# Optimization experiments

Hardware: AMD Instinct MI355X
Metric: run time of the kernel (lower is better)

Reference implementation:

```python
import jax, jax.numpy as jnp
import numpy as np
import math

N_CELLS = 16384
INPUT_DIM = 512
HIDDEN = 512


def build_neighbors(n):
    n_bits = max(1, int(math.ceil(math.log2(n))))
    idx = np.arange(n)
    flips = [idx ^ (1 << b) for b in range(n_bits)]
    ring = [(idx + 1) % n, (idx - 1) % n]
    allnb = np.stack(flips + ring, axis=1)
    # dedupe per row; for power-of-2 n every row has exactly n_bits+1 uniques
    rows = [sorted(set(r.tolist())) for r in allnb]
    return np.asarray(rows, dtype=np.int32)


def setup_inputs() -> dict:
    key = jax.random.key(0)
    ks = jax.random.split(key, 12)
    n, d, h = N_CELLS, INPUT_DIM, HIDDEN
    amp = jax.random.uniform(ks[0], (n, h)) * 0.5 + 0.5
    phase = jax.random.normal(ks[1], (n, h)) * 0.3 + (2 * math.pi * jnp.arange(n) / n)[:, None]
    return {
        "x": jax.random.normal(ks[2], (1, d), dtype=jnp.float32),
        "pump_W": jax.random.normal(ks[3], (n, d), dtype=jnp.float32) / np.sqrt(d),
        "pump_b": jax.random.normal(ks[4], (n,), dtype=jnp.float32) * 0.01,
        "dec_W": jax.random.normal(ks[5], (d, 2 * h), dtype=jnp.float32) / np.sqrt(2 * h),
        "dec_b": jax.random.normal(ks[6], (d,), dtype=jnp.float32) * 0.01,
        "cs_re": (amp * jnp.cos(phase)).astype(jnp.float32),
        "cs_im": (amp * jnp.sin(phase)).astype(jnp.float32),
        "excited": jax.random.uniform(ks[7], (n,)) * 0.6,  # some cells above 0.5 threshold
        "phase_vel": jax.random.normal(ks[8], (n, h), dtype=jnp.float32) * 0.05,
        "cav_re": jax.random.normal(ks[9], (h,), dtype=jnp.float32) * 0.01,
        "cav_im": jax.random.normal(ks[10], (h,), dtype=jnp.float32) * 0.01,
        "neighbors": jnp.asarray(build_neighbors(n)),
    }


def reference(x, pump_W, pump_b, dec_W, dec_b, cs_re, cs_im, excited, phase_vel, cav_re, cav_im, neighbors):
    states = (cs_re + 1j * cs_im).astype(jnp.complex64)          # [n,h]
    cavity = (cav_re + 1j * cav_im).astype(jnp.complex64)        # [h]

    # pump + excited fraction update
    pump = jax.nn.sigmoid(x @ pump_W.T + pump_b)[0]              # [n]
    excited = jnp.clip(excited * 0.95 + pump * 0.05, 0.0, 1.0)

    # free phase rotation: polar(1, 0.1*phase_vel)
    states = states * jnp.exp(1j * (phase_vel * 0.1)).astype(jnp.complex64)

    # neighbor phase coupling (hypercube + ring, k=15 neighbors each)
    ang = jnp.angle(states)                                      # [n,h]
    nb_states = states[neighbors]                                # [n,k,h]
    coupling = jnp.cos(ang[:, None, :] - ang[neighbors])         # [n,k,h]
    interference = 0.1 * jnp.sum(coupling * nb_states, axis=1)   # [n,h]
    k = neighbors.shape[1]
    new_states = 0.7 * states + 0.3 * interference / k

    # lasing: population inversion threshold
    lasing = excited > 0.5                                       # [n]
    n_lasing = jnp.sum(lasing)
    maskf = lasing.astype(jnp.float32)[:, None]
    # emission uses pre-phase-lock states (torch copies lasing_cells first)
    emission = jnp.sum(new_states * maskf, axis=0) / jnp.maximum(n_lasing, 1).astype(jnp.float32)
    cavity_new = jnp.where(n_lasing > 0, 0.8 * cavity + 0.2 * emission, cavity)

    # phase-lock lasing cells to (old) cavity phase
    cavity_phase = jnp.angle(cavity)                             # old cavity
    new_ang = jnp.angle(new_states)
    locked = 0.3 * cavity_phase[None, :] + 0.7 * new_ang
    locked_states = jnp.abs(new_states) * jnp.exp(1j * locked)
    new_states = jnp.where(lasing[:, None], locked_states.astype(jnp.complex64), new_states)
    excited = jnp.where(lasing, excited * 0.9, excited * 0.98)

    # cavity feedback (updated cavity) + amplitude renorm
    new_states = new_states + 0.05 * cavity_new[None, :]
    amp = jnp.abs(new_states)
    amp = amp / (jnp.max(amp, axis=-1, keepdims=True) + 1e-8)
    final_states = (amp * jnp.exp(1j * jnp.angle(new_states))).astype(jnp.complex64)

    # decode cavity mode
    out_real = jnp.concatenate([cavity_new.real, cavity_new.imag])[None, :].astype(jnp.float32)  # [1,2h]
    pred = out_real @ dec_W.T + dec_b                            # [1, input_dim]
    tension = jnp.var(jnp.abs(final_states))
    return pred, tension
```

## Files before the change

kernel.cpp:

```cpp
#include <hip/hip_runtime.h>
#include <hip/hip_fp16.h>
#include <math.h>

#define N_CELLS 16384
#define HID 512
#define IND 512
#define KNB 15
#define NCOPY 64

#define ROT_BLOCKS  8192
#define PUMP_BLOCKS 4096
#define ZERO_BLOCKS 64

#define CPB 32
#define CELL_BLOCKS (N_CELLS / CPB)
#define PRED_BLOCKS 128

#define CNT_OFF   0
#define EMIS_OFF  128
#define LAS_OFF   (EMIS_OFF + NCOPY*1024*4)
#define VPART_OFF (LAS_OFF + N_CELLS*4)
#define ROT_OFF   (1<<20)
#define NST_OFF   (ROT_OFF + (size_t)N_CELLS*HID*4)

__device__ inline __half2 f2h2(float f) { union { float f; __half2 h; } u; u.f = f; return u.h; }
__device__ inline float   h22f(__half2 h) { union { float f; __half2 h; } u; u.h = h; return u.f; }

__global__ __launch_bounds__(256) void k_front(const float* __restrict__ cr,
                                               const float* __restrict__ ci,
                                               const float* __restrict__ pv,
                                               float4* __restrict__ rot,
                                               const float* __restrict__ x,
                                               const float* __restrict__ pW,
                                               const float* __restrict__ pb,
                                               const float* __restrict__ excited,
                                               int* __restrict__ lasing,
                                               float* __restrict__ emis,
                                               int* __restrict__ cnt) {
    int b = blockIdx.x;
    int tid = threadIdx.x;
    if (b < ROT_BLOCKS) {
        int i = b * 256 + tid;
        const float4* cr4 = (const float4*)cr;
        const float4* ci4 = (const float4*)ci;
        const float4* pv4 = (const float4*)pv;
        float4 a = cr4[i], bb = ci4[i], t = pv4[i];
        float s0, c0, s1, c1, s2, c2, s3, c3;
        __sincosf(0.1f * t.x, &s0, &c0);
        __sincosf(0.1f * t.y, &s1, &c1);
        __sincosf(0.1f * t.z, &s2, &c2);
        __sincosf(0.1f * t.w, &s3, &c3);
        float re0 = a.x * c0 - bb.x * s0, im0 = a.x * s0 + bb.x * c0;
        float re1 = a.y * c1 - bb.y * s1, im1 = a.y * s1 + bb.y * c1;
        float re2 = a.z * c2 - bb.z * s2, im2 = a.z * s2 + bb.z * c2;
        float re3 = a.w * c3 - bb.w * s3, im3 = a.w * s3 + bb.w * c3;
        rot[i] = make_float4(h22f(__floats2half2_rn(re0, re1)),
                             h22f(__floats2half2_rn(im0, im1)),
                             h22f(__floats2half2_rn(re2, re3)),
                             h22f(__floats2half2_rn(im2, im3)));
    } else if (b < ROT_BLOCKS + PUMP_BLOCKS) {
        int gtid = (b - ROT_BLOCKS) * 256 + tid;
        int cell = gtid >> 6;
        int lane = gtid & 63;
        const float4* w4 = (const float4*)(pW + (size_t)cell * IND);
        const float4* x4 = (const float4*)x;
        float acc = 0.f;
#pragma unroll
        for (int t = 0; t < (IND / 4) / 64; ++t) {
            float4 a = w4[lane + 64 * t];
            float4 bx = x4[lane + 64 * t];
            acc += a.x * bx.x + a.y * bx.y + a.z * bx.z + a.w * bx.w;
        }
#pragma unroll
        for (int o = 32; o; o >>= 1) acc += __shfl_xor(acc, o, 64);
        if (lane == 0) {
            float p = 1.f / (1.f + expf(-(acc + pb[cell])));
            float e = excited[cell] * 0.95f + p * 0.05f;
            e = fminf(fmaxf(e, 0.f), 1.f);
            lasing[cell] = (e > 0.5f) ? 1 : 0;
        }
    } else {
        int zb = b - ROT_BLOCKS - PUMP_BLOCKS;
        int idx = zb * 256 + tid;
        ((float4*)emis)[idx] = make_float4(0.f, 0.f, 0.f, 0.f);
        if (zb == 0 && tid == 0) *cnt = 0;
    }
}

__global__ __launch_bounds__(256) void k_coup(const float2* __restrict__ rot2,
                                              const int* __restrict__ nbrs,
                                              const int* __restrict__ lasing,
                                              float2* __restrict__ nst2,
                                              float* __restrict__ emis) {
    __shared__ int nb[KNB];
    __shared__ int las;
    int cell = blockIdx.x;
    int tid = threadIdx.x;
    if (tid < KNB) nb[tid] = nbrs[cell * KNB + tid];
    if (tid == KNB) las = lasing[cell];
    __syncthreads();

    float2 raw = rot2[(size_t)cell * (HID / 2) + tid];
    __half2 sre = f2h2(raw.x), sim = f2h2(raw.y);
    float s0x = __low2float(sre), s1x = __high2float(sre);
    float s0y = __low2float(sim), s1y = __high2float(sim);
    float r0 = rsqrtf(s0x * s0x + s0y * s0y);
    float r1 = rsqrtf(s1x * s1x + s1y * s1y);

    __half2 are = __float2half2_rn(0.f), aim = __float2half2_rn(0.f);
#pragma unroll
    for (int t = 0; t < KNB; ++t) {
        float2 qraw = rot2[(size_t)nb[t] * (HID / 2) + tid];
        __half2 qre = f2h2(qraw.x), qim = f2h2(qraw.y);
        __half2 d  = __hfma2(sim, qim, __hmul2(sre, qre));
        __half2 qn = __hfma2(qim, qim, __hmul2(qre, qre));
        __half2 t2 = __hmul2(d, h2rsqrt(qn));
        are = __hfma2(t2, qre, are);
        aim = __hfma2(t2, qim, aim);
    }
    float ar0 = __low2float(are), ar1 = __high2float(are);
    float ai0 = __low2float(aim), ai1 = __high2float(aim);
    float k0 = 0.002f * r0, k1 = 0.002f * r1;
    float nr0 = 0.7f * s0x + k0 * ar0, ni0 = 0.7f * s0y + k0 * ai0;
    float nr1 = 0.7f * s1x + k1 * ar1, ni1 = 0.7f * s1y + k1 * ai1;
    nst2[(size_t)cell * (HID / 2) + tid] =
        make_float2(h22f(__floats2half2_rn(nr0, nr1)),
                    h22f(__floats2half2_rn(ni0, ni1)));
    if (las) {
        int c0 = tid << 1;
        float* em = emis + (size_t)(cell & (NCOPY - 1)) * 1024;
        atomicAdd(em + c0,     nr0); atomicAdd(em + 512 + c0,     ni0);
        atomicAdd(em + c0 + 1, nr1); atomicAdd(em + 512 + c0 + 1, ni1);
    }
}

__global__ __launch_bounds__(256) void k_finall(const float2* __restrict__ nst2,
                                                const int* __restrict__ lasv,
                                                const float* __restrict__ emis,
                                                const float* __restrict__ cavr,
                                                const float* __restrict__ cavi,
                                                const float* __restrict__ dW,
                                                const float* __restrict__ db,
                                                float2* __restrict__ vpart,
                                                int* __restrict__ cnt,
                                                float* __restrict__ out) {
    __shared__ float sout[1024];
    __shared__ float sphase[512];
    __shared__ int   ic[4];
    __shared__ int   snl;
    __shared__ float sred[4];
    __shared__ float sbc;
    __shared__ float w1[4], w2[4];
    __shared__ int   slast;

    int t = threadIdx.x;
    int wid = t >> 6, lane = t & 63;

    const int4* l4 = (const int4*)lasv;
    int n = 0;
#pragma unroll
    for (int k = 0; k < N_CELLS / 4 / 256; ++k) {
        int4 v = l4[t + 256 * k];
        n += v.x + v.y + v.z + v.w;
    }
#pragma unroll
    for (int o = 32; o; o >>= 1) n += __shfl_xor(n, o, 64);
    if (lane == 0) ic[wid] = n;

    float4 acc = make_float4(0.f, 0.f, 0.f, 0.f);
    const float4* e4 = (const float4*)emis;
#pragma unroll 8
    for (int k = 0; k < NCOPY; ++k) {
        float4 v = e4[k * 256 + t];
        acc.x += v.x; acc.y += v.y; acc.z += v.z; acc.w += v.w;
    }
    __syncthreads();
    if (t == 0) snl = ic[0] + ic[1] + ic[2] + ic[3];
    __syncthreads();
    int nl = snl;

    const float4* cr4 = (const float4*)cavr;
    const float4* ci4 = (const float4*)cavi;
    float4 cv = (t < 128) ? cr4[t] : ci4[t - 128];
    float4 nv;
    if (nl > 0) {
        float inv = 0.2f / (float)(nl > 1 ? nl : 1);
        nv = make_float4(0.8f * cv.x + acc.x * inv, 0.8f * cv.y + acc.y * inv,
                         0.8f * cv.z + acc.z * inv, 0.8f * cv.w + acc.w * inv);
    } else {
        nv = cv;
    }
    ((float4*)sout)[t] = nv;
    if (t < 128) {
        float4 cr = cr4[t], ci = ci4[t];
        sphase[4 * t]     = atan2f(ci.x, cr.x);
        sphase[4 * t + 1] = atan2f(ci.y, cr.y);
        sphase[4 * t + 2] = atan2f(ci.z, cr.z);
        sphase[4 * t + 3] = atan2f(ci.w, cr.w);
    }
    __syncthreads();

    int b = blockIdx.x;
    if (b < CELL_BLOCKS) {
        int c0 = t << 1;
        float fcr0 = 0.05f * sout[c0],       fcr1 = 0.05f * sout[c0 + 1];
        float fci0 = 0.05f * sout[512 + c0], fci1 = 0.05f * sout[512 + c0 + 1];
        float ph0 = sphase[c0], ph1 = sphase[c0 + 1];
        float s1 = 0.f, s2 = 0.f;
        for (int i = 0; i < CPB; ++i) {
            int cell = b * CPB + i;
            int las = lasv[cell];
            float2 raw = nst2[(size_t)cell * (HID / 2) + t];
            __half2 reh = f2h2(raw.x), imh = f2h2(raw.y);
            float vx0 = __low2float(reh), vx1 = __high2float(reh);
            float vy0 = __low2float(imh), vy1 = __high2float(imh);
            if (las) {
                float r0 = sqrtf(vx0 * vx0 + vy0 * vy0);
                float r1 = sqrtf(vx1 * vx1 + vy1 * vy1);
                float l0 = 0.3f * ph0 + 0.7f * atan2f(vy0, vx0);
                float l1 = 0.3f * ph1 + 0.7f * atan2f(vy1, vx1);
                float sn0, cs0, sn1, cs1;
                __sincosf(l0, &sn0, &cs0);
                __sincosf(l1, &sn1, &cs1);
                vx0 = r0 * cs0; vy0 = r0 * sn0;
                vx1 = r1 * cs1; vy1 = r1 * sn1;
            }
            vx0 += fcr0; vy0 += fci0;
            vx1 += fcr1; vy1 += fci1;
            float amp0 = sqrtf(vx0 * vx0 + vy0 * vy0);
            float amp1 = sqrtf(vx1 * vx1 + vy1 * vy1);
            float m = fmaxf(amp0, amp1);
#pragma unroll
            for (int o = 32; o; o >>= 1) m = fmaxf(m, __shfl_xor(m, o, 64));
            if (lane == 0) sred[wid] = m;
            __syncthreads();
            if (t == 0)
                sbc = fmaxf(fmaxf(sred[0], sred[1]), fmaxf(sred[2], sred[3]));
            __syncthreads();
            float inv = 1.f / (sbc + 1e-8f);
            float a0 = amp0 * inv, a1 = amp1 * inv;
            s1 += a0 + a1;
            s2 += a0 * a0 + a1 * a1;
        }
#pragma unroll
        for (int o = 32; o; o >>= 1) { s1 += __shfl_xor(s1, o, 64); s2 += __shfl_xor(s2, o, 64); }
        if (lane == 0) { w1[wid] = s1; w2[wid] = s2; }
        __syncthreads();
        if (t == 0) {
            vpart[b] = make_float2(w1[0] + w1[1] + w1[2] + w1[3],
                                   w2[0] + w2[1] + w2[2] + w2[3]);
            __threadfence();
            int old = atomicAdd(cnt, 1);
            slast = (old == CELL_BLOCKS - 1) ? 1 : 0;
        }
        __syncthreads();
        if (slast) {
            __threadfence();
            double d1 = (double)vpart[t].x + (double)vpart[t + 256].x;
            double d2 = (double)vpart[t].y + (double)vpart[t + 256].y;
#pragma unroll
            for (int o = 32; o; o >>= 1) { d1 += __shfl_xor(d1, o, 64); d2 += __shfl_xor(d2, o, 64); }
            __shared__ double l1s[4], l2s[4];
            if (lane == 0) { l1s[wid] = d1; l2s[wid] = d2; }
            __syncthreads();
            if (t == 0) {
                double t1 = l1s[0] + l1s[1] + l1s[2] + l1s[3];
                double t2 = l2s[0] + l2s[1] + l2s[2] + l2s[3];
                double nn = (double)N_CELLS * (double)HID;
                double mean = t1 / nn;
                out[IND] = (float)(t2 / nn - mean * mean);
            }
        }
    } else {
        int j = (b - CELL_BLOCKS) * 4 + wid;
        const float4* w4 = (const float4*)(dW + (size_t)j * (2 * HID));
        const float4* o4 = (const float4*)sout;
        float a2 = 0.f;
#pragma unroll
        for (int tt = 0; tt < 4; ++tt) {
            float4 a = w4[lane + 64 * tt];
            float4 bx = o4[lane + 64 * tt];
            a2 += a.x * bx.x + a.y * bx.y + a.z * bx.z + a.w * bx.w;
        }
#pragma unroll
        for (int o = 32; o; o >>= 1) a2 += __shfl_xor(a2, o, 64);
        if (lane == 0) out[j] = a2 + db[j];
    }
}

extern "C" void kernel_launch(void* const* d_in, const int* in_sizes, int n_in,
                              void* d_out, int out_size, void* d_ws, size_t ws_size,
                              hipStream_t stream) {
    const float* x       = (const float*)d_in[0];
    const float* pump_W  = (const float*)d_in[1];
    const float* pump_b  = (const float*)d_in[2];
    const float* dec_W   = (const float*)d_in[3];
    const float* dec_b   = (const float*)d_in[4];
    const float* cs_re   = (const float*)d_in[5];
    const float* cs_im   = (const float*)d_in[6];
    const float* excited = (const float*)d_in[7];
    const float* pvel    = (const float*)d_in[8];
    const float* cav_re  = (const float*)d_in[9];
    const float* cav_im  = (const float*)d_in[10];
    const int*   nbrs    = (const int*)d_in[11];

    float* out = (float*)d_out;
    char* ws = (char*)d_ws;
    int*    cnt   = (int*)(ws + CNT_OFF);
    float*  emis  = (float*)(ws + EMIS_OFF);
    int*    lasv  = (int*)(ws + LAS_OFF);
    float2* vpart = (float2*)(ws + VPART_OFF);
    float2* rot2  = (float2*)(ws + ROT_OFF);
    float2* nst2  = (float2*)(ws + NST_OFF);

    k_front<<<ROT_BLOCKS + PUMP_BLOCKS + ZERO_BLOCKS, 256, 0, stream>>>(
        cs_re, cs_im, pvel, (float4*)rot2, x, pump_W, pump_b, excited, lasv, emis, cnt);
    k_coup<<<N_CELLS, 256, 0, stream>>>(rot2, nbrs, lasv, nst2, emis);
    k_finall<<<CELL_BLOCKS + PRED_BLOCKS, 256, 0, stream>>>(
        nst2, lasv, emis, cav_re, cav_im, dec_W, dec_b, vpart, cnt, out);
}
```

Baseline: 266.8 us.

## Prescale states by inverse sqrt amplitude and assign one wave per cell in final pass

The front kernel now stores each rotated state scaled by 1/sqrt(|s|). With that scaling the coupling loop no longer needs a per-neighbor half-precision rsqrt, and the own-cell magnitude is recovered algebraically. The final kernel is restructured so each 64-lane wave handles whole cells with float4 loads, which replaces the per-cell block-wide max reduction and its two __syncthreads with a wave shuffle reduction. The fp16 intermediate now holds differently scaled values, which may change rounding behaviour.

```diff
diff --git a/kernel.cpp b/kernel.cpp
--- a/kernel.cpp
+++ b/kernel.cpp
@@ -29,7 +29,7 @@
 __global__ __launch_bounds__(256) void k_front(const float* __restrict__ cr,
                                                const float* __restrict__ ci,
                                                const float* __restrict__ pv,
-                                               float4* __restrict__ rot,
+                                               float4* __restrict__ yout,
                                                const float* __restrict__ x,
                                                const float* __restrict__ pW,
                                                const float* __restrict__ pb,
@@ -45,19 +45,23 @@
         const float4* ci4 = (const float4*)ci;
         const float4* pv4 = (const float4*)pv;
         float4 a = cr4[i], bb = ci4[i], t = pv4[i];
+        float sc0 = rsqrtf(sqrtf(a.x * a.x + bb.x * bb.x));
+        float sc1 = rsqrtf(sqrtf(a.y * a.y + bb.y * bb.y));
+        float sc2 = rsqrtf(sqrtf(a.z * a.z + bb.z * bb.z));
+        float sc3 = rsqrtf(sqrtf(a.w * a.w + bb.w * bb.w));
         float s0, c0, s1, c1, s2, c2, s3, c3;
         __sincosf(0.1f * t.x, &s0, &c0);
         __sincosf(0.1f * t.y, &s1, &c1);
         __sincosf(0.1f * t.z, &s2, &c2);
         __sincosf(0.1f * t.w, &s3, &c3);
-        float re0 = a.x * c0 - bb.x * s0, im0 = a.x * s0 + bb.x * c0;
-        float re1 = a.y * c1 - bb.y * s1, im1 = a.y * s1 + bb.y * c1;
-        float re2 = a.z * c2 - bb.z * s2, im2 = a.z * s2 + bb.z * c2;
-        float re3 = a.w * c3 - bb.w * s3, im3 = a.w * s3 + bb.w * c3;
-        rot[i] = make_float4(h22f(__floats2half2_rn(re0, re1)),
-                             h22f(__floats2half2_rn(im0, im1)),
-                             h22f(__floats2half2_rn(re2, re3)),
-                             h22f(__floats2half2_rn(im2, im3)));
+        float re0 = (a.x * c0 - bb.x * s0) * sc0, im0 = (a.x * s0 + bb.x * c0) * sc0;
+        float re1 = (a.y * c1 - bb.y * s1) * sc1, im1 = (a.y * s1 + bb.y * c1) * sc1;
+        float re2 = (a.z * c2 - bb.z * s2) * sc2, im2 = (a.z * s2 + bb.z * c2) * sc2;
+        float re3 = (a.w * c3 - bb.w * s3) * sc3, im3 = (a.w * s3 + bb.w * c3) * sc3;
+        yout[i] = make_float4(h22f(__floats2half2_rn(re0, re1)),
+                              h22f(__floats2half2_rn(im0, im1)),
+                              h22f(__floats2half2_rn(re2, re3)),
+                              h22f(__floats2half2_rn(im2, im3)));
     } else if (b < ROT_BLOCKS + PUMP_BLOCKS) {
         int gtid = (b - ROT_BLOCKS) * 256 + tid;
         int cell = gtid >> 6;
@@ -87,7 +91,7 @@
     }
 }
 
-__global__ __launch_bounds__(256) void k_coup(const float2* __restrict__ rot2,
+__global__ __launch_bounds__(256) void k_coup(const float2* __restrict__ y2,
                                               const int* __restrict__ nbrs,
                                               const int* __restrict__ lasing,
                                               float2* __restrict__ nst2,
@@ -100,38 +104,62 @@
     if (tid == KNB) las = lasing[cell];
     __syncthreads();
 
-    float2 raw = rot2[(size_t)cell * (HID / 2) + tid];
-    __half2 sre = f2h2(raw.x), sim = f2h2(raw.y);
-    float s0x = __low2float(sre), s1x = __high2float(sre);
-    float s0y = __low2float(sim), s1y = __high2float(sim);
-    float r0 = rsqrtf(s0x * s0x + s0y * s0y);
-    float r1 = rsqrtf(s1x * s1x + s1y * s1y);
+    float2 raw = y2[(size_t)cell * (HID / 2) + tid];
+    __half2 yre = f2h2(raw.x), yim = f2h2(raw.y);
+    float y0x = __low2float(yre), y1x = __high2float(yre);
+    float y0y = __low2float(yim), y1y = __high2float(yim);
+    float a0 = y0x * y0x + y0y * y0y;
+    float a1 = y1x * y1x + y1y * y1y;
 
     __half2 are = __float2half2_rn(0.f), aim = __float2half2_rn(0.f);
 #pragma unroll
     for (int t = 0; t < KNB; ++t) {
-        float2 qraw = rot2[(size_t)nb[t] * (HID / 2) + tid];
-        __half2 qre = f2h2(qraw.x), qim = f2h2(qraw.y);
-        __half2 d  = __hfma2(sim, qim, __hmul2(sre, qre));
-        __half2 qn = __hfma2(qim, qim, __hmul2(qre, qre));
-        __half2 t2 = __hmul2(d, h2rsqrt(qn));
-        are = __hfma2(t2, qre, are);
-        aim = __hfma2(t2, qim, aim);
-    }
-    float ar0 = __low2float(are), ar1 = __high2float(are);
-    float ai0 = __low2float(aim), ai1 = __high2float(aim);
-    float k0 = 0.002f * r0, k1 = 0.002f * r1;
-    float nr0 = 0.7f * s0x + k0 * ar0, ni0 = 0.7f * s0y + k0 * ai0;
-    float nr1 = 0.7f * s1x + k1 * ar1, ni1 = 0.7f * s1y + k1 * ai1;
+        float2 q = y2[(size_t)nb[t] * (HID / 2) + tid];
+        __half2 qre = f2h2(q.x), qim = f2h2(q.y);
+        __half2 d = __hfma2(yim, qim, __hmul2(yre, qre));
+        are = __hfma2(d, qre, are);
+        aim = __hfma2(d, qim, aim);
+    }
+    float rs0 = rsqrtf(a0), rs1 = rsqrtf(a1);
+    float sq0 = a0 * rs0, sq1 = a1 * rs1;
+    float c0 = 0.7f * sq0, c1 = 0.7f * sq1;
+    float k0 = 0.002f * rs0, k1 = 0.002f * rs1;
+    float nr0 = c0 * y0x + k0 * __low2float(are);
+    float ni0 = c0 * y0y + k0 * __low2float(aim);
+    float nr1 = c1 * y1x + k1 * __high2float(are);
+    float ni1 = c1 * y1y + k1 * __high2float(aim);
     nst2[(size_t)cell * (HID / 2) + tid] =
         make_float2(h22f(__floats2half2_rn(nr0, nr1)),
                     h22f(__floats2half2_rn(ni0, ni1)));
     if (las) {
-        int c0 = tid << 1;
+        int c0i = tid << 1;
         float* em = emis + (size_t)(cell & (NCOPY - 1)) * 1024;
-        atomicAdd(em + c0,     nr0); atomicAdd(em + 512 + c0,     ni0);
-        atomicAdd(em + c0 + 1, nr1); atomicAdd(em + 512 + c0 + 1, ni1);
-    }
+        atomicAdd(em + c0i,     nr0); atomicAdd(em + 512 + c0i,     ni0);
+        atomicAdd(em + c0i + 1, nr1); atomicAdd(em + 512 + c0i + 1, ni1);
+    }
+}
+
+__device__ inline void chan2(float reh_f, float imh_f, int lasc,
+                             float cr0, float cr1, float ci0, float ci1,
+                             float p0, float p1, float& amp0, float& amp1) {
+    __half2 reh = f2h2(reh_f), imh = f2h2(imh_f);
+    float vx0 = __low2float(reh), vx1 = __high2float(reh);
+    float vy0 = __low2float(imh), vy1 = __high2float(imh);
+    if (lasc) {
+        float r0 = sqrtf(vx0 * vx0 + vy0 * vy0);
+        float r1 = sqrtf(vx1 * vx1 + vy1 * vy1);
+        float l0 = 0.3f * p0 + 0.7f * atan2f(vy0, vx0);
+        float l1 = 0.3f * p1 + 0.7f * atan2f(vy1, vx1);
+        float sn0, cs0, sn1, cs1;
+        __sincosf(l0, &sn0, &cs0);
+        __sincosf(l1, &sn1, &cs1);
+        vx0 = r0 * cs0; vy0 = r0 * sn0;
+        vx1 = r1 * cs1; vy1 = r1 * sn1;
+    }
+    vx0 += 0.05f * cr0; vy0 += 0.05f * ci0;
+    vx1 += 0.05f * cr1; vy1 += 0.05f * ci1;
+    amp0 = sqrtf(vx0 * vx0 + vy0 * vy0);
+    amp1 = sqrtf(vx1 * vx1 + vy1 * vy1);
 }
 
 __global__ __launch_bounds__(256) void k_finall(const float2* __restrict__ nst2,
@@ -148,8 +176,6 @@
     __shared__ float sphase[512];
     __shared__ int   ic[4];
     __shared__ int   snl;
-    __shared__ float sred[4];
-    __shared__ float sbc;
     __shared__ float w1[4], w2[4];
     __shared__ int   slast;
 
@@ -202,45 +228,34 @@
 
     int b = blockIdx.x;
     if (b < CELL_BLOCKS) {
-        int c0 = t << 1;
-        float fcr0 = 0.05f * sout[c0],       fcr1 = 0.05f * sout[c0 + 1];
-        float fci0 = 0.05f * sout[512 + c0], fci1 = 0.05f * sout[512 + c0 + 1];
-        float ph0 = sphase[c0], ph1 = sphase[c0 + 1];
+        float4 cA = ((float4*)sout)[lane];
+        float4 cB = ((float4*)sout)[lane + 64];
+        float4 dA = ((float4*)sout)[128 + lane];
+        float4 dB = ((float4*)sout)[128 + 64 + lane];
+        float4 pA = ((float4*)sphase)[lane];
+        float4 pB = ((float4*)sphase)[lane + 64];
         float s1 = 0.f, s2 = 0.f;
-        for (int i = 0; i < CPB; ++i) {
-            int cell = b * CPB + i;
-            int las = lasv[cell];
-            float2 raw = nst2[(size_t)cell * (HID / 2) + t];
-            __half2 reh = f2h2(raw.x), imh = f2h2(raw.y);
-            float vx0 = __low2float(reh), vx1 = __high2float(reh);
-            float vy0 = __low2float(imh), vy1 = __high2float(imh);
-            if (las) {
-                float r0 = sqrtf(vx0 * vx0 + vy0 * vy0);
-                float r1 = sqrtf(vx1 * vx1 + vy1 * vy1);
-                float l0 = 0.3f * ph0 + 0.7f * atan2f(vy0, vx0);
-                float l1 = 0.3f * ph1 + 0.7f * atan2f(vy1, vx1);
-                float sn0, cs0, sn1, cs1;
-                __sincosf(l0, &sn0, &cs0);
-                __sincosf(l1, &sn1, &cs1);
-                vx0 = r0 * cs0; vy0 = r0 * sn0;
-                vx1 = r1 * cs1; vy1 = r1 * sn1;
-            }
-            vx0 += fcr0; vy0 += fci0;
-            vx1 += fcr1; vy1 += fci1;
-            float amp0 = sqrtf(vx0 * vx0 + vy0 * vy0);
-            float amp1 = sqrtf(vx1 * vx1 + vy1 * vy1);
-            float m = fmaxf(amp0, amp1);
-#pragma unroll
-            for (int o = 32; o; o >>= 1) m = fmaxf(m, __shfl_xor(m, o, 64));
-            if (lane == 0) sred[wid] = m;
-            __syncthreads();
-            if (t == 0)
-                sbc = fmaxf(fmaxf(sred[0], sred[1]), fmaxf(sred[2], sred[3]));
-            __syncthreads();
-            float inv = 1.f / (sbc + 1e-8f);
-            float a0 = amp0 * inv, a1 = amp1 * inv;
-            s1 += a0 + a1;
-            s2 += a0 * a0 + a1 * a1;
+#pragma unroll 2
+        for (int i = 0; i < CPB / 4; ++i) {
+            int cell = b * CPB + wid * (CPB / 4) + i;
+            int lasc = lasv[cell];
+            const float4* nrow = (const float4*)nst2 + (size_t)cell * 128;
+            float4 A = nrow[lane], B = nrow[lane + 64];
+            float m0, m1, m2, m3, m4, m5, m6, m7;
+            chan2(A.x, A.y, lasc, cA.x, cA.y, dA.x, dA.y, pA.x, pA.y, m0, m1);
+            chan2(A.z, A.w, lasc, cA.z, cA.w, dA.z, dA.w, pA.z, pA.w, m2, m3);
+            chan2(B.x, B.y, lasc, cB.x, cB.y, dB.x, dB.y, pB.x, pB.y, m4, m5);
+            chan2(B.z, B.w, lasc, cB.z, cB.w, dB.z, dB.w, pB.z, pB.w, m6, m7);
+            float mx = fmaxf(fmaxf(fmaxf(m0, m1), fmaxf(m2, m3)),
+                             fmaxf(fmaxf(m4, m5), fmaxf(m6, m7)));
+#pragma unroll
+            for (int o = 32; o; o >>= 1) mx = fmaxf(mx, __shfl_xor(mx, o, 64));
+            float inv = 1.f / (mx + 1e-8f);
+            float a0 = m0 * inv, a1 = m1 * inv, a2 = m2 * inv, a3 = m3 * inv;
+            float a4 = m4 * inv, a5 = m5 * inv, a6 = m6 * inv, a7 = m7 * inv;
+            s1 += (a0 + a1) + (a2 + a3) + (a4 + a5) + (a6 + a7);
+            s2 += (a0 * a0 + a1 * a1) + (a2 * a2 + a3 * a3)
+                + (a4 * a4 + a5 * a5) + (a6 * a6 + a7 * a7);
         }
 #pragma unroll
         for (int o = 32; o; o >>= 1) { s1 += __shfl_xor(s1, o, 64); s2 += __shfl_xor(s2, o, 64); }
@@ -310,12 +325,12 @@
     float*  emis  = (float*)(ws + EMIS_OFF);
     int*    lasv  = (int*)(ws + LAS_OFF);
     float2* vpart = (float2*)(ws + VPART_OFF);
-    float2* rot2  = (float2*)(ws + ROT_OFF);
+    float2* y2    = (float2*)(ws + ROT_OFF);
     float2* nst2  = (float2*)(ws + NST_OFF);
 
     k_front<<<ROT_BLOCKS + PUMP_BLOCKS + ZERO_BLOCKS, 256, 0, stream>>>(
-        cs_re, cs_im, pvel, (float4*)rot2, x, pump_W, pump_b, excited, lasv, emis, cnt);
-    k_coup<<<N_CELLS, 256, 0, stream>>>(rot2, nbrs, lasv, nst2, emis);
+        cs_re, cs_im, pvel, (float4*)y2, x, pump_W, pump_b, excited, lasv, emis, cnt);
+    k_coup<<<N_CELLS, 256, 0, stream>>>(y2, nbrs, lasv, nst2, emis);
     k_finall<<<CELL_BLOCKS + PRED_BLOCKS, 256, 0, stream>>>(
         nst2, lasv, emis, cav_re, cav_im, dec_W, dec_b, vpart, cnt, out);
 }
```

Measured after the change: 253.0 us. 5.2% less time.
